# Optimization experiments

Measured on AMD Instinct MI355X. Metric: run time of the kernel, lower is better.

Reference implementation:

```python
import jax, jax.numpy as jnp
import numpy as np

D_MODEL = 1024
N_HEADS = 16
D_K = D_MODEL // N_HEADS
THETA = 10000.0
BATCH = 1
SEQ = 4096


def setup_inputs() -> dict:
    key = jax.random.key(0)
    ks = jax.random.split(key, 5)
    std = (2.0 / (D_MODEL + D_MODEL)) ** 0.5
    mk = lambda k: jax.random.truncated_normal(k, -3.0, 3.0, (D_MODEL, D_MODEL), jnp.float32) * std
    return {
        "x": jax.random.normal(ks[0], (BATCH, SEQ, D_MODEL), jnp.float32),
        "Wq": mk(ks[1]),
        "Wk": mk(ks[2]),
        "Wv": mk(ks[3]),
        "Wo": mk(ks[4]),
    }


def _rope(x, pos, inv_freq):
    # x: [b, h, s, d_k]; pos: [s]; inv_freq: [d_k/2]
    angles = pos[:, None].astype(jnp.float32) * inv_freq  # [s, d_k/2]
    cos = jnp.repeat(jnp.cos(angles), 2, axis=-1)  # [s, d_k]
    sin = jnp.repeat(jnp.sin(angles), 2, axis=-1)
    # interleaved rotation: (-x1, x0, -x3, x2, ...)
    x_rot = jnp.stack([-x[..., 1::2], x[..., 0::2]], axis=-1).reshape(x.shape)
    return x * cos + x_rot * sin


def reference(x, Wq, Wk, Wv, Wo):
    b, s, _ = x.shape
    h, dk = N_HEADS, D_K
    proj = lambda W: jnp.einsum('bsi,oi->bso', x, W).reshape(b, s, h, dk).transpose(0, 2, 1, 3)
    q = proj(Wq)
    k = proj(Wk)
    v = proj(Wv)
    pos = jnp.arange(s)
    inv_freq = 1.0 / THETA ** (jnp.arange(0, dk, 2, dtype=jnp.float32) / dk)
    q = _rope(q, pos, inv_freq)
    k = _rope(k, pos, inv_freq)
    scores = jnp.einsum('bhqd,bhkd->bhqk', q, k) / jnp.sqrt(jnp.asarray(dk, jnp.float32))
    causal_mask = jnp.arange(s)[None, :] > jnp.arange(s)[:, None]  # [s, s], True above diag
    scores = jnp.where(causal_mask, -jnp.inf, scores)
    weights = jax.nn.softmax(scores, axis=-1)
    out = jnp.einsum('bhqk,bhkd->bhqd', weights, v)
    out = out.transpose(0, 2, 1, 3).reshape(b, s, h * dk)
    return jnp.einsum('bsi,oi->bso', out, Wo)
```

## Files before the change

### kernel.cpp

```cpp
#include <hip/hip_runtime.h>
#include <hip/hip_bf16.h>


typedef __hip_bfloat16 bf16;
using s16x4 = __attribute__((ext_vector_type(4))) short;
using s16x8 = __attribute__((ext_vector_type(8))) short;
using f32x4 = __attribute__((ext_vector_type(4))) float;

#define SEQ 4096
#define DMODEL 1024
#define NHEADS 16
#define DK 64
#define LOG2_THETA 13.287712379549449f
#define SCALE_LOG2E 0.1803368801111244f

__device__ __forceinline__ void async16(const bf16* g, bf16* l) {
  __builtin_amdgcn_global_load_lds(
      (const __attribute__((address_space(1))) unsigned int*)g,
      (__attribute__((address_space(3))) unsigned int*)l, 16, 0, 0);
}

__global__ __launch_bounds__(256)
void conv_kernel(const float* __restrict__ s0, const float* __restrict__ s1,
                 const float* __restrict__ s2, const float* __restrict__ s3,
                 const float* __restrict__ s4,
                 bf16* __restrict__ d0, bf16* __restrict__ d1,
                 bf16* __restrict__ d2, bf16* __restrict__ d3,
                 bf16* __restrict__ d4) {
  const int z = blockIdx.z;
  const float* s = (z == 0) ? s0 : (z == 1) ? s1 : (z == 2) ? s2 : (z == 3) ? s3 : s4;
  bf16* d = (z == 0) ? d0 : (z == 1) ? d1 : (z == 2) ? d2 : (z == 3) ? d3 : d4;
  const int n = (z == 0) ? SEQ * DMODEL : DMODEL * DMODEL;
  const int i = (blockIdx.x * 256 + threadIdx.x) * 8;
  if (i >= n) return;
  const float4 a = *(const float4*)(s + i);
  const float4 b = *(const float4*)(s + i + 4);
  union { bf16 h[8]; s16x8 v; } u;
  u.h[0] = __float2bfloat16(a.x); u.h[1] = __float2bfloat16(a.y);
  u.h[2] = __float2bfloat16(a.z); u.h[3] = __float2bfloat16(a.w);
  u.h[4] = __float2bfloat16(b.x); u.h[5] = __float2bfloat16(b.y);
  u.h[6] = __float2bfloat16(b.z); u.h[7] = __float2bfloat16(b.w);
  *(s16x8*)(d + i) = u.v;
}

__global__ __launch_bounds__(256)
void gemm_kernel(const bf16* __restrict__ A,
                 const bf16* __restrict__ W0, const bf16* __restrict__ W1,
                 const bf16* __restrict__ W2,
                 bf16* __restrict__ D0, bf16* __restrict__ D1,
                 bf16* __restrict__ D2, float* __restrict__ Df,
                 int mode_base) {
  const int mode = mode_base + (int)blockIdx.z;
  const bf16* __restrict__ W = (mode == 1) ? W1 : (mode == 2) ? W2 : W0;
  bf16* __restrict__ D = (mode == 1) ? D1 : (mode == 2) ? D2 : D0;

  const int tid  = threadIdx.x;
  const int lane = tid & 63;
  const int wave = tid >> 6;
  const int wm = wave >> 1, wn = wave & 1;
  const int quad = lane >> 4, l16 = lane & 15;
  const int m0 = blockIdx.x * 128;
  const int n0 = blockIdx.y * 128;

  __shared__ __align__(16) bf16 As[128 * 32];
  __shared__ __align__(16) bf16 Bs[128 * 32];
  __shared__ __align__(16) bf16 Es[4][64 * 64];

  f32x4 acc[4][4] = {};

  const int ldrow = lane >> 2;
  const int ldcol = (lane & 3) * 8;

  for (int k0 = 0; k0 < DMODEL; k0 += 32) {
#pragma unroll
    for (int c = 0; c < 2; ++c) {
      const int chunk = wave * 2 + c;
      const int row = chunk * 16 + ldrow;
      async16(&A[(size_t)(m0 + row) * DMODEL + k0 + ldcol], &As[chunk * 512]);
      async16(&W[(size_t)(n0 + row) * DMODEL + k0 + ldcol], &Bs[chunk * 512]);
    }
    __syncthreads();

    s16x8 af[4], bfr[4];
#pragma unroll
    for (int i = 0; i < 4; ++i)
      af[i] = *(const s16x8*)&As[(wm * 64 + i * 16 + l16) * 32 + quad * 8];
#pragma unroll
    for (int j = 0; j < 4; ++j)
      bfr[j] = *(const s16x8*)&Bs[(wn * 64 + j * 16 + l16) * 32 + quad * 8];
#pragma unroll
    for (int i = 0; i < 4; ++i)
#pragma unroll
      for (int j = 0; j < 4; ++j)
        acc[i][j] = __builtin_amdgcn_mfma_f32_16x16x32_bf16(af[i], bfr[j],
                                                            acc[i][j], 0, 0, 0);
    __syncthreads();
  }

  if (mode == 3) {
#pragma unroll
    for (int i = 0; i < 4; ++i)
#pragma unroll
      for (int j = 0; j < 4; ++j) {
        const int col = n0 + wn * 64 + j * 16 + l16;
#pragma unroll
        for (int r = 0; r < 4; ++r) {
          const int srow = m0 + wm * 64 + i * 16 + quad * 4 + r;
          Df[(size_t)srow * DMODEL + col] = acc[i][j][r];
        }
      }
    return;
  }

  if (mode == 2) {
#pragma unroll
    for (int i = 0; i < 4; ++i)
#pragma unroll
      for (int j = 0; j < 4; ++j)
#pragma unroll
        for (int r = 0; r < 4; ++r)
          Es[wave][(j * 16 + l16) * 64 + i * 16 + quad * 4 + r] =
              __float2bfloat16(acc[i][j][r]);
  } else {
#pragma unroll
    for (int i = 0; i < 4; ++i)
#pragma unroll
      for (int j = 0; j < 4; ++j)
#pragma unroll
        for (int r = 0; r < 4; ++r)
          Es[wave][(i * 16 + quad * 4 + r) * 64 + j * 16 + l16] =
              __float2bfloat16(acc[i][j][r]);
  }
  __syncthreads();

  const int h = (n0 >> 6) + wn;
  const int g  = lane >> 3;
  const int c8 = (lane & 7) * 8;

  if (mode == 2) {
#pragma unroll
    for (int t = 0; t < 8; ++t) {
      const int d = t * 8 + g;
      const s16x8 v = *(const s16x8*)&Es[wave][d * 64 + c8];
      *(s16x8*)&D[((size_t)h * DK + d) * SEQ + m0 + wm * 64 + c8] = v;
    }
  } else {
    const float qs = (mode == 0) ? SCALE_LOG2E : 1.0f;
    float sn[4], cs[4], s8[4], c8r[4], invf[4];
    const int srow0 = m0 + wm * 64 + g;
#pragma unroll
    for (int k = 0; k < 4; ++k) {
      const int p = (c8 >> 1) + k;
      invf[k] = __builtin_amdgcn_exp2f((float)p * (-2.0f / 64.0f) * LOG2_THETA);
      sincosf((float)srow0 * invf[k], &sn[k], &cs[k]);
      sincosf(8.0f * invf[k], &s8[k], &c8r[k]);
      sn[k] *= qs; cs[k] *= qs;
    }
#pragma unroll
    for (int t = 0; t < 8; ++t) {
      const int rl = t * 8 + g;
      union { bf16 h[8]; s16x8 v; } u, o;
      u.v = *(const s16x8*)&Es[wave][rl * 64 + c8];
#pragma unroll
      for (int k = 0; k < 4; ++k) {
        const float x0 = __bfloat162float(u.h[2 * k]);
        const float x1 = __bfloat162float(u.h[2 * k + 1]);
        o.h[2 * k]     = __float2bfloat16(x0 * cs[k] - x1 * sn[k]);
        o.h[2 * k + 1] = __float2bfloat16(x1 * cs[k] + x0 * sn[k]);
        const float ns_ = sn[k] * c8r[k] + cs[k] * s8[k];
        cs[k] = cs[k] * c8r[k] - sn[k] * s8[k];
        sn[k] = ns_;
      }
      const int srow = m0 + wm * 64 + rl;
      *(s16x8*)&D[((size_t)h * SEQ + srow) * DK + c8] = o.v;
    }
  }
}

#define PTP 72
__global__ __launch_bounds__(256, 2)
void attn_kernel(const bf16* __restrict__ Q, const bf16* __restrict__ K,
                 const bf16* __restrict__ Vt, bf16* __restrict__ O) {
  const int tid  = threadIdx.x;
  const int lane = tid & 63;
  const int wave = tid >> 6;
  const int quad = lane >> 4, l16 = lane & 15;
  const int pr = blockIdx.x;
  const int h = blockIdx.y;
  const bf16* __restrict__ Qh = Q + (size_t)h * SEQ * DK;
  const bf16* __restrict__ Kh = K + (size_t)h * SEQ * DK;
  const bf16* __restrict__ Vh = Vt + (size_t)h * DK * SEQ;

  __shared__ __align__(16) bf16 Ks[2][64 * 64];
  __shared__ __align__(16) bf16 Vs[2][64 * 64];
  __shared__ __align__(16) bf16 Pt[4][16 * PTP];
  bf16* __restrict__ Ptw = Pt[wave];

  const short ONE = 0x3F80;
  const s16x8 ones = {ONE, ONE, ONE, ONE, ONE, ONE, ONE, ONE};

  const int srow = lane >> 3;
  const int schk = (lane & 7) ^ srow;
  const int xsw  = l16 & 7;

#pragma unroll
  for (int phase = 0; phase < 2; ++phase) {
    const int qb = phase ? pr : 63 - pr;
    const int q0 = qb * 64;
    const int qw = q0 + wave * 16;
    const int nb = qb + 1;

    const s16x8 aq0 = *(const s16x8*)&Qh[(size_t)(qw + l16) * DK + quad * 8];
    const s16x8 aq1 = *(const s16x8*)&Qh[(size_t)(qw + l16) * DK + 32 + quad * 8];

    f32x4 oacc[4] = {};
    f32x4 lacc = {};

    {
      const bf16* kg = Kh;
#pragma unroll
      for (int c = 0; c < 2; ++c) {
        const int chunk = wave * 2 + c;
        async16(kg + (size_t)(chunk * 8 + srow) * 64 + schk * 8,
                &Ks[0][chunk * 512]);
        async16(Vh + (size_t)(chunk * 8 + srow) * SEQ + schk * 8,
                &Vs[0][chunk * 512]);
      }
    }
    __syncthreads();

    for (int kb = 0; kb < nb; ++kb) {
      const int cur = kb & 1;
      if (kb + 1 < nb) {
        const int nxt = cur ^ 1;
        const int kv1 = (kb + 1) * 64;
        const bf16* kg = Kh + (size_t)kv1 * DK;
#pragma unroll
        for (int c = 0; c < 2; ++c) {
          const int chunk = wave * 2 + c;
          async16(kg + (size_t)(chunk * 8 + srow) * 64 + schk * 8,
                  &Ks[nxt][chunk * 512]);
          async16(Vh + (size_t)(chunk * 8 + srow) * SEQ + kv1 + schk * 8,
                  &Vs[nxt][chunk * 512]);
        }
      }

      f32x4 sc[4] = {};
      __builtin_amdgcn_s_setprio(1);
#pragma unroll
      for (int hh = 0; hh < 4; ++hh) {
        const bf16* kr = &Ks[cur][(hh * 16 + l16) * 64];
        const s16x8 ak0 = *(const s16x8*)&kr[(quad ^ xsw) * 8];
        const s16x8 ak1 = *(const s16x8*)&kr[((quad + 4) ^ xsw) * 8];
        sc[hh] = __builtin_amdgcn_mfma_f32_16x16x32_bf16(ak0, aq0, sc[hh], 0, 0, 0);
        sc[hh] = __builtin_amdgcn_mfma_f32_16x16x32_bf16(ak1, aq1, sc[hh], 0, 0, 0);
      }
      __builtin_amdgcn_s_setprio(0);

      if (kb == nb - 1) {
        const int lim = wave * 16 + l16 - quad * 4;
#pragma unroll
        for (int hh = 0; hh < 4; ++hh)
#pragma unroll
          for (int r = 0; r < 4; ++r)
            if (hh * 16 + r > lim) sc[hh][r] = -1e30f;
      }

#pragma unroll
      for (int hh = 0; hh < 4; ++hh) {
        union { bf16 b[4]; s16x4 v; } pk;
#pragma unroll
        for (int r = 0; r < 4; ++r)
          pk.b[r] = __float2bfloat16(__builtin_amdgcn_exp2f(sc[hh][r]));
        *(s16x4*)&Ptw[l16 * PTP + hh * 16 + quad * 4] = pk.v;
      }
      const s16x8 ap0 = *(const s16x8*)&Ptw[l16 * PTP + quad * 8];
      const s16x8 ap1 = *(const s16x8*)&Ptw[l16 * PTP + 32 + quad * 8];

      __builtin_amdgcn_s_setprio(1);
#pragma unroll
      for (int ns = 0; ns < 4; ++ns) {
        const bf16* vr = &Vs[cur][(ns * 16 + l16) * 64];
        const s16x8 bv0 = *(const s16x8*)&vr[(quad ^ xsw) * 8];
        const s16x8 bv1 = *(const s16x8*)&vr[((quad + 4) ^ xsw) * 8];
        oacc[ns] = __builtin_amdgcn_mfma_f32_16x16x32_bf16(ap0, bv0, oacc[ns], 0, 0, 0);
        oacc[ns] = __builtin_amdgcn_mfma_f32_16x16x32_bf16(ap1, bv1, oacc[ns], 0, 0, 0);
      }
      lacc = __builtin_amdgcn_mfma_f32_16x16x32_bf16(ap0, ones, lacc, 0, 0, 0);
      lacc = __builtin_amdgcn_mfma_f32_16x16x32_bf16(ap1, ones, lacc, 0, 0, 0);
      __builtin_amdgcn_s_setprio(0);

      __syncthreads();
    }

    float rl[4];
#pragma unroll
    for (int r = 0; r < 4; ++r) rl[r] = __builtin_amdgcn_rcpf(lacc[r]);
#pragma unroll
    for (int ns = 0; ns < 4; ++ns)
#pragma unroll
      for (int r = 0; r < 4; ++r)
        Ptw[(quad * 4 + r) * PTP + ns * 16 + l16] =
            __float2bfloat16(oacc[ns][r] * rl[r]);
    const int g = lane >> 3, c8 = (lane & 7) * 8;
#pragma unroll
    for (int t = 0; t < 2; ++t) {
      const int row = t * 8 + g;
      const s16x8 v = *(const s16x8*)&Ptw[row * PTP + c8];
      *(s16x8*)&O[(size_t)(qw + row) * DMODEL + h * DK + c8] = v;
    }
    __syncthreads();
  }
}

extern "C" void kernel_launch(void* const* d_in, const int* in_sizes, int n_in,
                              void* d_out, int out_size, void* d_ws, size_t ws_size,
                              hipStream_t stream) {
  const float* x  = (const float*)d_in[0];
  const float* Wq = (const float*)d_in[1];
  const float* Wk = (const float*)d_in[2];
  const float* Wv = (const float*)d_in[3];
  const float* Wo = (const float*)d_in[4];
  float* out = (float*)d_out;

  bf16* ws = (bf16*)d_ws;
  bf16* xb   = ws;
  bf16* Wqb  = xb  + (size_t)SEQ * DMODEL;
  bf16* Wkb  = Wqb + (size_t)DMODEL * DMODEL;
  bf16* Wvb  = Wkb + (size_t)DMODEL * DMODEL;
  bf16* Wob  = Wvb + (size_t)DMODEL * DMODEL;
  bf16* Qb   = Wob + (size_t)DMODEL * DMODEL;
  bf16* Kb   = Qb  + (size_t)SEQ * DMODEL;
  bf16* Vtb  = Kb  + (size_t)SEQ * DMODEL;
  bf16* Attn = Vtb + (size_t)SEQ * DMODEL;

  conv_kernel<<<dim3(SEQ * DMODEL / (256 * 8), 1, 5), 256, 0, stream>>>(
      x, Wq, Wk, Wv, Wo, xb, Wqb, Wkb, Wvb, Wob);
  gemm_kernel<<<dim3(SEQ / 128, DMODEL / 128, 3), 256, 0, stream>>>(
      xb, Wqb, Wkb, Wvb, Qb, Kb, Vtb, out, 0);
  attn_kernel<<<dim3(32, NHEADS), 256, 0, stream>>>(Qb, Kb, Vtb, Attn);
  gemm_kernel<<<dim3(SEQ / 128, DMODEL / 128, 1), 256, 0, stream>>>(
      Attn, Wob, Wob, Wob, Attn, Attn, Attn, out, 3);
}
```

Before: 225.4 us.

## Split attention into one block per query tile with heavy-first scheduling

```diff
diff --git a/kernel.cpp b/kernel.cpp
--- a/kernel.cpp
+++ b/kernel.cpp
@@ -177,23 +177,28 @@
   }
 }
 
-#define PTP 72
-__global__ __launch_bounds__(256, 2)
+__global__ __launch_bounds__(256, 4)
 void attn_kernel(const bf16* __restrict__ Q, const bf16* __restrict__ K,
                  const bf16* __restrict__ Vt, bf16* __restrict__ O) {
   const int tid  = threadIdx.x;
   const int lane = tid & 63;
   const int wave = tid >> 6;
   const int quad = lane >> 4, l16 = lane & 15;
-  const int pr = blockIdx.x;
-  const int h = blockIdx.y;
+
+  const int i  = (int)blockIdx.x;
+  const int j  = i & 255;
+  const int vv = 3 - (i >> 8);
+  const int h  = j & 15;
+  const int a  = j >> 4;
+  const int qb = vv * 16 + ((vv & 1) ? (15 - a) : a);
+
   const bf16* __restrict__ Qh = Q + (size_t)h * SEQ * DK;
   const bf16* __restrict__ Kh = K + (size_t)h * SEQ * DK;
   const bf16* __restrict__ Vh = Vt + (size_t)h * DK * SEQ;
 
   __shared__ __align__(16) bf16 Ks[2][64 * 64];
   __shared__ __align__(16) bf16 Vs[2][64 * 64];
-  __shared__ __align__(16) bf16 Pt[4][16 * PTP];
+  __shared__ __align__(16) bf16 Pt[4][16 * 64];
   bf16* __restrict__ Ptw = Pt[wave];
 
   const short ONE = 0x3F80;
@@ -202,114 +207,112 @@
   const int srow = lane >> 3;
   const int schk = (lane & 7) ^ srow;
   const int xsw  = l16 & 7;
-
-#pragma unroll
-  for (int phase = 0; phase < 2; ++phase) {
-    const int qb = phase ? pr : 63 - pr;
-    const int q0 = qb * 64;
-    const int qw = q0 + wave * 16;
-    const int nb = qb + 1;
-
-    const s16x8 aq0 = *(const s16x8*)&Qh[(size_t)(qw + l16) * DK + quad * 8];
-    const s16x8 aq1 = *(const s16x8*)&Qh[(size_t)(qw + l16) * DK + 32 + quad * 8];
-
-    f32x4 oacc[4] = {};
-    f32x4 lacc = {};
-
-    {
-      const bf16* kg = Kh;
+  const int xp   = (l16 & 7) << 3;
+
+  const int q0 = qb * 64;
+  const int qw = q0 + wave * 16;
+  const int nb = qb + 1;
+
+  const s16x8 aq0 = *(const s16x8*)&Qh[(size_t)(qw + l16) * DK + quad * 8];
+  const s16x8 aq1 = *(const s16x8*)&Qh[(size_t)(qw + l16) * DK + 32 + quad * 8];
+
+  f32x4 oacc[4] = {};
+  f32x4 lacc = {};
+
+  {
+    const bf16* kg = Kh;
+#pragma unroll
+    for (int c = 0; c < 2; ++c) {
+      const int chunk = wave * 2 + c;
+      async16(kg + (size_t)(chunk * 8 + srow) * 64 + schk * 8,
+              &Ks[0][chunk * 512]);
+      async16(Vh + (size_t)(chunk * 8 + srow) * SEQ + schk * 8,
+              &Vs[0][chunk * 512]);
+    }
+  }
+  __syncthreads();
+
+  for (int kb = 0; kb < nb; ++kb) {
+    const int cur = kb & 1;
+    if (kb + 1 < nb) {
+      const int nxt = cur ^ 1;
+      const int kv1 = (kb + 1) * 64;
+      const bf16* kg = Kh + (size_t)kv1 * DK;
 #pragma unroll
       for (int c = 0; c < 2; ++c) {
         const int chunk = wave * 2 + c;
         async16(kg + (size_t)(chunk * 8 + srow) * 64 + schk * 8,
-                &Ks[0][chunk * 512]);
-        async16(Vh + (size_t)(chunk * 8 + srow) * SEQ + schk * 8,
-                &Vs[0][chunk * 512]);
+                &Ks[nxt][chunk * 512]);
+        async16(Vh + (size_t)(chunk * 8 + srow) * SEQ + kv1 + schk * 8,
+                &Vs[nxt][chunk * 512]);
       }
     }
+
+    f32x4 sc[4] = {};
+    __builtin_amdgcn_s_setprio(1);
+#pragma unroll
+    for (int hh = 0; hh < 4; ++hh) {
+      const bf16* kr = &Ks[cur][(hh * 16 + l16) * 64];
+      const s16x8 ak0 = *(const s16x8*)&kr[(quad ^ xsw) * 8];
+      const s16x8 ak1 = *(const s16x8*)&kr[((quad + 4) ^ xsw) * 8];
+      sc[hh] = __builtin_amdgcn_mfma_f32_16x16x32_bf16(ak0, aq0, sc[hh], 0, 0, 0);
+      sc[hh] = __builtin_amdgcn_mfma_f32_16x16x32_bf16(ak1, aq1, sc[hh], 0, 0, 0);
+    }
+    __builtin_amdgcn_s_setprio(0);
+
+    if (kb == nb - 1) {
+      const int lim = wave * 16 + l16 - quad * 4;
+#pragma unroll
+      for (int hh = 0; hh < 4; ++hh)
+#pragma unroll
+        for (int r = 0; r < 4; ++r)
+          if (hh * 16 + r > lim) sc[hh][r] = -1e30f;
+    }
+
+#pragma unroll
+    for (int hh = 0; hh < 4; ++hh) {
+      union { bf16 b[4]; s16x4 v; } pk;
+#pragma unroll
+      for (int r = 0; r < 4; ++r)
+        pk.b[r] = __float2bfloat16(__builtin_amdgcn_exp2f(sc[hh][r]));
+      *(s16x4*)&Ptw[l16 * 64 + ((hh * 16 + quad * 4) ^ xp)] = pk.v;
+    }
+    const s16x8 ap0 = *(const s16x8*)&Ptw[l16 * 64 + ((quad * 8) ^ xp)];
+    const s16x8 ap1 = *(const s16x8*)&Ptw[l16 * 64 + ((32 + quad * 8) ^ xp)];
+
+    __builtin_amdgcn_s_setprio(1);
+#pragma unroll
+    for (int ns = 0; ns < 4; ++ns) {
+      const bf16* vr = &Vs[cur][(ns * 16 + l16) * 64];
+      const s16x8 bv0 = *(const s16x8*)&vr[(quad ^ xsw) * 8];
+      const s16x8 bv1 = *(const s16x8*)&vr[((quad + 4) ^ xsw) * 8];
+      oacc[ns] = __builtin_amdgcn_mfma_f32_16x16x32_bf16(ap0, bv0, oacc[ns], 0, 0, 0);
+      oacc[ns] = __builtin_amdgcn_mfma_f32_16x16x32_bf16(ap1, bv1, oacc[ns], 0, 0, 0);
+    }
+    lacc = __builtin_amdgcn_mfma_f32_16x16x32_bf16(ap0, ones, lacc, 0, 0, 0);
+    lacc = __builtin_amdgcn_mfma_f32_16x16x32_bf16(ap1, ones, lacc, 0, 0, 0);
+    __builtin_amdgcn_s_setprio(0);
+
     __syncthreads();
-
-    for (int kb = 0; kb < nb; ++kb) {
-      const int cur = kb & 1;
-      if (kb + 1 < nb) {
-        const int nxt = cur ^ 1;
-        const int kv1 = (kb + 1) * 64;
-        const bf16* kg = Kh + (size_t)kv1 * DK;
-#pragma unroll
-        for (int c = 0; c < 2; ++c) {
-          const int chunk = wave * 2 + c;
-          async16(kg + (size_t)(chunk * 8 + srow) * 64 + schk * 8,
-                  &Ks[nxt][chunk * 512]);
-          async16(Vh + (size_t)(chunk * 8 + srow) * SEQ + kv1 + schk * 8,
-                  &Vs[nxt][chunk * 512]);
-        }
-      }
-
-      f32x4 sc[4] = {};
-      __builtin_amdgcn_s_setprio(1);
-#pragma unroll
-      for (int hh = 0; hh < 4; ++hh) {
-        const bf16* kr = &Ks[cur][(hh * 16 + l16) * 64];
-        const s16x8 ak0 = *(const s16x8*)&kr[(quad ^ xsw) * 8];
-        const s16x8 ak1 = *(const s16x8*)&kr[((quad + 4) ^ xsw) * 8];
-        sc[hh] = __builtin_amdgcn_mfma_f32_16x16x32_bf16(ak0, aq0, sc[hh], 0, 0, 0);
-        sc[hh] = __builtin_amdgcn_mfma_f32_16x16x32_bf16(ak1, aq1, sc[hh], 0, 0, 0);
-      }
-      __builtin_amdgcn_s_setprio(0);
-
-      if (kb == nb - 1) {
-        const int lim = wave * 16 + l16 - quad * 4;
-#pragma unroll
-        for (int hh = 0; hh < 4; ++hh)
-#pragma unroll
-          for (int r = 0; r < 4; ++r)
-            if (hh * 16 + r > lim) sc[hh][r] = -1e30f;
-      }
-
-#pragma unroll
-      for (int hh = 0; hh < 4; ++hh) {
-        union { bf16 b[4]; s16x4 v; } pk;
-#pragma unroll
-        for (int r = 0; r < 4; ++r)
-          pk.b[r] = __float2bfloat16(__builtin_amdgcn_exp2f(sc[hh][r]));
-        *(s16x4*)&Ptw[l16 * PTP + hh * 16 + quad * 4] = pk.v;
-      }
-      const s16x8 ap0 = *(const s16x8*)&Ptw[l16 * PTP + quad * 8];
-      const s16x8 ap1 = *(const s16x8*)&Ptw[l16 * PTP + 32 + quad * 8];
-
-      __builtin_amdgcn_s_setprio(1);
-#pragma unroll
-      for (int ns = 0; ns < 4; ++ns) {
-        const bf16* vr = &Vs[cur][(ns * 16 + l16) * 64];
-        const s16x8 bv0 = *(const s16x8*)&vr[(quad ^ xsw) * 8];
-        const s16x8 bv1 = *(const s16x8*)&vr[((quad + 4) ^ xsw) * 8];
-        oacc[ns] = __builtin_amdgcn_mfma_f32_16x16x32_bf16(ap0, bv0, oacc[ns], 0, 0, 0);
-        oacc[ns] = __builtin_amdgcn_mfma_f32_16x16x32_bf16(ap1, bv1, oacc[ns], 0, 0, 0);
-      }
-      lacc = __builtin_amdgcn_mfma_f32_16x16x32_bf16(ap0, ones, lacc, 0, 0, 0);
-      lacc = __builtin_amdgcn_mfma_f32_16x16x32_bf16(ap1, ones, lacc, 0, 0, 0);
-      __builtin_amdgcn_s_setprio(0);
-
-      __syncthreads();
-    }
-
-    float rl[4];
-#pragma unroll
-    for (int r = 0; r < 4; ++r) rl[r] = __builtin_amdgcn_rcpf(lacc[r]);
-#pragma unroll
-    for (int ns = 0; ns < 4; ++ns)
-#pragma unroll
-      for (int r = 0; r < 4; ++r)
-        Ptw[(quad * 4 + r) * PTP + ns * 16 + l16] =
-            __float2bfloat16(oacc[ns][r] * rl[r]);
-    const int g = lane >> 3, c8 = (lane & 7) * 8;
-#pragma unroll
-    for (int t = 0; t < 2; ++t) {
-      const int row = t * 8 + g;
-      const s16x8 v = *(const s16x8*)&Ptw[row * PTP + c8];
-      *(s16x8*)&O[(size_t)(qw + row) * DMODEL + h * DK + c8] = v;
-    }
-    __syncthreads();
+  }
+
+  float rl[4];
+#pragma unroll
+  for (int r = 0; r < 4; ++r) rl[r] = __builtin_amdgcn_rcpf(lacc[r]);
+#pragma unroll
+  for (int ns = 0; ns < 4; ++ns)
+#pragma unroll
+    for (int r = 0; r < 4; ++r) {
+      const int row = quad * 4 + r;
+      Ptw[row * 64 + ((ns * 16 + l16) ^ ((row & 7) << 3))] =
+          __float2bfloat16(oacc[ns][r] * rl[r]);
+    }
+  const int g = lane >> 3, c8 = (lane & 7) * 8;
+#pragma unroll
+  for (int t = 0; t < 2; ++t) {
+    const int row = t * 8 + g;
+    const s16x8 v = *(const s16x8*)&Ptw[row * 64 + (c8 ^ ((row & 7) << 3))];
+    *(s16x8*)&O[(size_t)(qw + row) * DMODEL + h * DK + c8] = v;
   }
 }
 
@@ -338,7 +341,7 @@
       x, Wq, Wk, Wv, Wo, xb, Wqb, Wkb, Wvb, Wob);
   gemm_kernel<<<dim3(SEQ / 128, DMODEL / 128, 3), 256, 0, stream>>>(
       xb, Wqb, Wkb, Wvb, Qb, Kb, Vtb, out, 0);
-  attn_kernel<<<dim3(32, NHEADS), 256, 0, stream>>>(Qb, Kb, Vtb, Attn);
+  attn_kernel<<<dim3(64 * NHEADS), 256, 0, stream>>>(Qb, Kb, Vtb, Attn);
   gemm_kernel<<<dim3(SEQ / 128, DMODEL / 128, 1), 256, 0, stream>>>(
       Attn, Wob, Wob, Wob, Attn, Attn, Attn, out, 3);
 }
```

After: 218.9 us. 2.9% less time.

## Double attention query tile per wave and schedule heavy causal blocks first

Applied to the files above, without the earlier changes.

```diff
diff --git a/kernel.cpp b/kernel.cpp
--- a/kernel.cpp
+++ b/kernel.cpp
@@ -185,15 +185,20 @@
   const int lane = tid & 63;
   const int wave = tid >> 6;
   const int quad = lane >> 4, l16 = lane & 15;
-  const int pr = blockIdx.x;
-  const int h = blockIdx.y;
+
+  const int i  = (int)blockIdx.x;
+  const int j  = i & 255;
+  const int h  = j & 15;
+  const int a  = j >> 4;
+  const int qb = (i < 256) ? (31 - a) : a;
+
   const bf16* __restrict__ Qh = Q + (size_t)h * SEQ * DK;
   const bf16* __restrict__ Kh = K + (size_t)h * SEQ * DK;
   const bf16* __restrict__ Vh = Vt + (size_t)h * DK * SEQ;
 
   __shared__ __align__(16) bf16 Ks[2][64 * 64];
   __shared__ __align__(16) bf16 Vs[2][64 * 64];
-  __shared__ __align__(16) bf16 Pt[4][16 * PTP];
+  __shared__ __align__(16) bf16 Pt[4][32 * PTP];
   bf16* __restrict__ Ptw = Pt[wave];
 
   const short ONE = 0x3F80;
@@ -203,113 +208,133 @@
   const int schk = (lane & 7) ^ srow;
   const int xsw  = l16 & 7;
 
-#pragma unroll
-  for (int phase = 0; phase < 2; ++phase) {
-    const int qb = phase ? pr : 63 - pr;
-    const int q0 = qb * 64;
-    const int qw = q0 + wave * 16;
-    const int nb = qb + 1;
-
-    const s16x8 aq0 = *(const s16x8*)&Qh[(size_t)(qw + l16) * DK + quad * 8];
-    const s16x8 aq1 = *(const s16x8*)&Qh[(size_t)(qw + l16) * DK + 32 + quad * 8];
-
-    f32x4 oacc[4] = {};
-    f32x4 lacc = {};
-
-    {
-      const bf16* kg = Kh;
+  const int q0 = qb * 128;
+  const int qw = q0 + wave * 32;
+  const int nb = 2 * qb + 2;
+
+  s16x8 aq[2][2];
+#pragma unroll
+  for (int g = 0; g < 2; ++g) {
+    const size_t qr = (size_t)(qw + g * 16 + l16) * DK;
+    aq[g][0] = *(const s16x8*)&Qh[qr + quad * 8];
+    aq[g][1] = *(const s16x8*)&Qh[qr + 32 + quad * 8];
+  }
+
+  f32x4 oacc[2][4] = {};
+  f32x4 lacc[2] = {};
+
+  {
+    const bf16* kg = Kh;
+#pragma unroll
+    for (int c = 0; c < 2; ++c) {
+      const int chunk = wave * 2 + c;
+      async16(kg + (size_t)(chunk * 8 + srow) * 64 + schk * 8,
+              &Ks[0][chunk * 512]);
+      async16(Vh + (size_t)(chunk * 8 + srow) * SEQ + schk * 8,
+              &Vs[0][chunk * 512]);
+    }
+  }
+  __syncthreads();
+
+  for (int kb = 0; kb < nb; ++kb) {
+    const int cur = kb & 1;
+    if (kb + 1 < nb) {
+      const int nxt = cur ^ 1;
+      const int kv1 = (kb + 1) * 64;
+      const bf16* kg = Kh + (size_t)kv1 * DK;
 #pragma unroll
       for (int c = 0; c < 2; ++c) {
         const int chunk = wave * 2 + c;
         async16(kg + (size_t)(chunk * 8 + srow) * 64 + schk * 8,
-                &Ks[0][chunk * 512]);
-        async16(Vh + (size_t)(chunk * 8 + srow) * SEQ + schk * 8,
-                &Vs[0][chunk * 512]);
-      }
-    }
-    __syncthreads();
-
-    for (int kb = 0; kb < nb; ++kb) {
-      const int cur = kb & 1;
-      if (kb + 1 < nb) {
-        const int nxt = cur ^ 1;
-        const int kv1 = (kb + 1) * 64;
-        const bf16* kg = Kh + (size_t)kv1 * DK;
-#pragma unroll
-        for (int c = 0; c < 2; ++c) {
-          const int chunk = wave * 2 + c;
-          async16(kg + (size_t)(chunk * 8 + srow) * 64 + schk * 8,
-                  &Ks[nxt][chunk * 512]);
-          async16(Vh + (size_t)(chunk * 8 + srow) * SEQ + kv1 + schk * 8,
-                  &Vs[nxt][chunk * 512]);
-        }
-      }
-
-      f32x4 sc[4] = {};
-      __builtin_amdgcn_s_setprio(1);
-#pragma unroll
-      for (int hh = 0; hh < 4; ++hh) {
-        const bf16* kr = &Ks[cur][(hh * 16 + l16) * 64];
-        const s16x8 ak0 = *(const s16x8*)&kr[(quad ^ xsw) * 8];
-        const s16x8 ak1 = *(const s16x8*)&kr[((quad + 4) ^ xsw) * 8];
-        sc[hh] = __builtin_amdgcn_mfma_f32_16x16x32_bf16(ak0, aq0, sc[hh], 0, 0, 0);
-        sc[hh] = __builtin_amdgcn_mfma_f32_16x16x32_bf16(ak1, aq1, sc[hh], 0, 0, 0);
-      }
-      __builtin_amdgcn_s_setprio(0);
-
-      if (kb == nb - 1) {
-        const int lim = wave * 16 + l16 - quad * 4;
+                &Ks[nxt][chunk * 512]);
+        async16(Vh + (size_t)(chunk * 8 + srow) * SEQ + kv1 + schk * 8,
+                &Vs[nxt][chunk * 512]);
+      }
+    }
+
+    f32x4 sc[2][4] = {};
+    __builtin_amdgcn_s_setprio(1);
+#pragma unroll
+    for (int hh = 0; hh < 4; ++hh) {
+      const bf16* kr = &Ks[cur][(hh * 16 + l16) * 64];
+      const s16x8 ak0 = *(const s16x8*)&kr[(quad ^ xsw) * 8];
+      const s16x8 ak1 = *(const s16x8*)&kr[((quad + 4) ^ xsw) * 8];
+#pragma unroll
+      for (int g = 0; g < 2; ++g) {
+        sc[g][hh] = __builtin_amdgcn_mfma_f32_16x16x32_bf16(ak0, aq[g][0], sc[g][hh], 0, 0, 0);
+        sc[g][hh] = __builtin_amdgcn_mfma_f32_16x16x32_bf16(ak1, aq[g][1], sc[g][hh], 0, 0, 0);
+      }
+    }
+    __builtin_amdgcn_s_setprio(0);
+
+    if (kb >= nb - 2) {
+      const int rel = (kb - (nb - 2)) * 64;
+#pragma unroll
+      for (int g = 0; g < 2; ++g) {
+        const int lim = wave * 32 + g * 16 + l16 - rel - quad * 4;
 #pragma unroll
         for (int hh = 0; hh < 4; ++hh)
 #pragma unroll
           for (int r = 0; r < 4; ++r)
-            if (hh * 16 + r > lim) sc[hh][r] = -1e30f;
-      }
-
+            if (hh * 16 + r > lim) sc[g][hh][r] = -1e30f;
+      }
+    }
+
+    s16x8 ap[2][2];
+#pragma unroll
+    for (int g = 0; g < 2; ++g) {
 #pragma unroll
       for (int hh = 0; hh < 4; ++hh) {
         union { bf16 b[4]; s16x4 v; } pk;
 #pragma unroll
         for (int r = 0; r < 4; ++r)
-          pk.b[r] = __float2bfloat16(__builtin_amdgcn_exp2f(sc[hh][r]));
-        *(s16x4*)&Ptw[l16 * PTP + hh * 16 + quad * 4] = pk.v;
-      }
-      const s16x8 ap0 = *(const s16x8*)&Ptw[l16 * PTP + quad * 8];
-      const s16x8 ap1 = *(const s16x8*)&Ptw[l16 * PTP + 32 + quad * 8];
-
-      __builtin_amdgcn_s_setprio(1);
-#pragma unroll
-      for (int ns = 0; ns < 4; ++ns) {
-        const bf16* vr = &Vs[cur][(ns * 16 + l16) * 64];
-        const s16x8 bv0 = *(const s16x8*)&vr[(quad ^ xsw) * 8];
-        const s16x8 bv1 = *(const s16x8*)&vr[((quad + 4) ^ xsw) * 8];
-        oacc[ns] = __builtin_amdgcn_mfma_f32_16x16x32_bf16(ap0, bv0, oacc[ns], 0, 0, 0);
-        oacc[ns] = __builtin_amdgcn_mfma_f32_16x16x32_bf16(ap1, bv1, oacc[ns], 0, 0, 0);
-      }
-      lacc = __builtin_amdgcn_mfma_f32_16x16x32_bf16(ap0, ones, lacc, 0, 0, 0);
-      lacc = __builtin_amdgcn_mfma_f32_16x16x32_bf16(ap1, ones, lacc, 0, 0, 0);
-      __builtin_amdgcn_s_setprio(0);
-
-      __syncthreads();
-    }
-
+          pk.b[r] = __float2bfloat16(__builtin_amdgcn_exp2f(sc[g][hh][r]));
+        *(s16x4*)&Ptw[(g * 16 + l16) * PTP + hh * 16 + quad * 4] = pk.v;
+      }
+      ap[g][0] = *(const s16x8*)&Ptw[(g * 16 + l16) * PTP + quad * 8];
+      ap[g][1] = *(const s16x8*)&Ptw[(g * 16 + l16) * PTP + 32 + quad * 8];
+    }
+
+    __builtin_amdgcn_s_setprio(1);
+#pragma unroll
+    for (int ns = 0; ns < 4; ++ns) {
+      const bf16* vr = &Vs[cur][(ns * 16 + l16) * 64];
+      const s16x8 bv0 = *(const s16x8*)&vr[(quad ^ xsw) * 8];
+      const s16x8 bv1 = *(const s16x8*)&vr[((quad + 4) ^ xsw) * 8];
+#pragma unroll
+      for (int g = 0; g < 2; ++g) {
+        oacc[g][ns] = __builtin_amdgcn_mfma_f32_16x16x32_bf16(ap[g][0], bv0, oacc[g][ns], 0, 0, 0);
+        oacc[g][ns] = __builtin_amdgcn_mfma_f32_16x16x32_bf16(ap[g][1], bv1, oacc[g][ns], 0, 0, 0);
+      }
+    }
+#pragma unroll
+    for (int g = 0; g < 2; ++g) {
+      lacc[g] = __builtin_amdgcn_mfma_f32_16x16x32_bf16(ap[g][0], ones, lacc[g], 0, 0, 0);
+      lacc[g] = __builtin_amdgcn_mfma_f32_16x16x32_bf16(ap[g][1], ones, lacc[g], 0, 0, 0);
+    }
+    __builtin_amdgcn_s_setprio(0);
+
+    __syncthreads();
+  }
+
+#pragma unroll
+  for (int g = 0; g < 2; ++g) {
     float rl[4];
 #pragma unroll
-    for (int r = 0; r < 4; ++r) rl[r] = __builtin_amdgcn_rcpf(lacc[r]);
+    for (int r = 0; r < 4; ++r) rl[r] = __builtin_amdgcn_rcpf(lacc[g][r]);
 #pragma unroll
     for (int ns = 0; ns < 4; ++ns)
 #pragma unroll
       for (int r = 0; r < 4; ++r)
-        Ptw[(quad * 4 + r) * PTP + ns * 16 + l16] =
-            __float2bfloat16(oacc[ns][r] * rl[r]);
-    const int g = lane >> 3, c8 = (lane & 7) * 8;
-#pragma unroll
-    for (int t = 0; t < 2; ++t) {
-      const int row = t * 8 + g;
-      const s16x8 v = *(const s16x8*)&Ptw[row * PTP + c8];
-      *(s16x8*)&O[(size_t)(qw + row) * DMODEL + h * DK + c8] = v;
-    }
-    __syncthreads();
+        Ptw[(g * 16 + quad * 4 + r) * PTP + ns * 16 + l16] =
+            __float2bfloat16(oacc[g][ns][r] * rl[r]);
+  }
+  const int g8 = lane >> 3, c8 = (lane & 7) * 8;
+#pragma unroll
+  for (int t = 0; t < 4; ++t) {
+    const int row = t * 8 + g8;
+    const s16x8 v = *(const s16x8*)&Ptw[row * PTP + c8];
+    *(s16x8*)&O[(size_t)(qw + row) * DMODEL + h * DK + c8] = v;
   }
 }
 
@@ -338,7 +363,7 @@
       x, Wq, Wk, Wv, Wo, xb, Wqb, Wkb, Wvb, Wob);
   gemm_kernel<<<dim3(SEQ / 128, DMODEL / 128, 3), 256, 0, stream>>>(
       xb, Wqb, Wkb, Wvb, Qb, Kb, Vtb, out, 0);
-  attn_kernel<<<dim3(32, NHEADS), 256, 0, stream>>>(Qb, Kb, Vtb, Attn);
+  attn_kernel<<<dim3(32 * NHEADS), 256, 0, stream>>>(Qb, Kb, Vtb, Attn);
   gemm_kernel<<<dim3(SEQ / 128, DMODEL / 128, 1), 256, 0, stream>>>(
       Attn, Wob, Wob, Wob, Attn, Attn, Attn, out, 3);
 }
```

Result: no change. 228.9 us (+1.5%).
